# Optimization experiments

Measured on AMD Instinct MI355X. Metric: run time of the kernel, lower is better.

The kernel has to match this reference:

```python
import jax, jax.numpy as jnp
import numpy as np

N, M, D, O = 16384, 4096, 256, 256

def setup_inputs() -> dict:
    key = jax.random.key(0)
    k1, k2, k3, k4, k5, k6, k7 = jax.random.split(key, 7)
    H_fine = jax.random.normal(k1, (N, D), dtype=jnp.float32)
    H_coarse = jax.random.normal(k2, (M, D), dtype=jnp.float32)
    inter_channel_adj = jax.random.randint(k3, (N, M), 0, 2).astype(jnp.float32)
    # attention = nn.Linear(2D, 1): weight vector [2D], bias scalar
    wa = jax.random.normal(k4, (2 * D,), dtype=jnp.float32) * (1.0 / np.sqrt(2 * D))
    ba = jax.random.normal(k5, (1,), dtype=jnp.float32) * 0.01
    # transform = nn.Linear(D, O), xavier_uniform weight
    lim = np.sqrt(6.0 / (D + O)).astype(np.float32)
    Wt = jax.random.uniform(k6, (O, D), minval=-lim, maxval=lim, dtype=jnp.float32)
    bt = jax.random.normal(k7, (O,), dtype=jnp.float32) * 0.01
    return {"H_fine": H_fine, "H_coarse": H_coarse,
            "inter_channel_adj": inter_channel_adj,
            "wa": wa, "ba": ba, "Wt": Wt, "bt": bt}

def reference(H_fine, H_coarse, inter_channel_adj, wa, ba, Wt, bt):
    d = H_fine.shape[-1]
    # additive attention: score_ij = [hf_i ; hc_j] . wa + b
    # = hf_i . wa[:d] + hc_j . wa[d:] + b  (avoids [N,M,2D] concat)
    sf = H_fine @ wa[:d]            # [N]
    sc = H_coarse @ wa[d:]          # [M]
    scores = sf[:, None] + sc[None, :] + ba[0]        # [N, M]
    masked = scores * inter_channel_adj               # [N, M]
    weights = jax.nn.softmax(masked, axis=-1)         # [N, M]
    attn_out = weights @ H_coarse                     # [N, D]
    attn_out = attn_out + H_fine                      # add_self=True
    out = attn_out @ Wt.T + bt                        # [N, O]
    return jax.nn.relu(out)
```

## Files before the change

### kernel.cpp

```cpp
#include <hip/hip_runtime.h>
#include <hip/hip_bf16.h>
#include <stdint.h>

#define N_ 16384
#define M_ 4096
#define D_ 256
#define O_ 256

#define WS_T    0
#define WS_U    65536
#define WS_R    81920
#define WS_WTP  98304
#define WS_BP   229376

typedef float  f32x4  __attribute__((ext_vector_type(4)));
typedef short  short8 __attribute__((ext_vector_type(8)));

__device__ __forceinline__ unsigned short f2bf(float f) {
  uint32_t u = __float_as_uint(f);
  u += 0x7FFFu + ((u >> 16) & 1u);
  return (unsigned short)(u >> 16);
}
__device__ __forceinline__ uint32_t cvtpk(float a, float b) {
  __hip_bfloat162 h = __float22bfloat162_rn(float2{a, b});
  uint32_t u;
  __builtin_memcpy(&u, &h, 4);
  return u;
}

__global__ __launch_bounds__(256) void prep_kernel(
    const float* __restrict__ Hf, const float* __restrict__ Hc,
    const float* __restrict__ wa, const float* __restrict__ ba,
    const float* __restrict__ Wt, float* __restrict__ tv,
    float* __restrict__ uv, unsigned short* __restrict__ BP,
    unsigned short* __restrict__ WtP, float* __restrict__ Rv) {
  __shared__ float tile[64][65];
  __shared__ float red[4][64];
  int b = blockIdx.x;
  int t = threadIdx.x;
  if (b < 5120) {
    int wv = t >> 6, lane = t & 63;
    const float* X; const float* w; const float* bias; float* outv; int row;
    if (b < 4096) { X = Hf; w = wa;      bias = ba;      outv = tv; row = b * 4 + wv; }
    else          { X = Hc; w = wa + D_; bias = nullptr; outv = uv; row = (b - 4096) * 4 + wv; }
    const float4* x4 = (const float4*)(X + (size_t)row * D_);
    const float4* w4 = (const float4*)w;
    float4 xa = x4[lane], wa4 = w4[lane];
    float s = xa.x * wa4.x + xa.y * wa4.y + xa.z * wa4.z + xa.w * wa4.w;
#pragma unroll
    for (int off = 32; off > 0; off >>= 1) s += __shfl_xor(s, off);
    if (lane == 0) outv[row] = expf(s + (bias ? bias[0] : 0.0f));
  } else if (b < 5376) {
    int bb = b - 5120;
    int bk = bb >> 2;
    int bc = bb & 3;
    int k0 = bk * 64, col0 = bc * 64;
    int lane = t & 63, wv = t >> 6;
    int m = lane & 15, q = lane >> 4;
    float colsum = 0.0f;
#pragma unroll
    for (int i = 0; i < 16; ++i) {
      int e = t + 256 * i;
      int kk = e >> 6, cc = e & 63;
      float v = Hc[(size_t)(k0 + kk) * D_ + col0 + cc];
      tile[kk][cc] = v;
      colsum += v;
    }
    red[wv][t & 63] = colsum;
    __syncthreads();
    if (t < 64)
      atomicAdd(&Rv[col0 + t], red[0][t] + red[1][t] + red[2][t] + red[3][t]);
#pragma unroll
    for (int t8 = 0; t8 < 2; ++t8) {
      int tile_id = t8 * 4 + wv;
      int sub = tile_id >> 2, g = tile_id & 3;
      int kgg = bk * 2 + sub;
      int cgg = bc * 4 + g;
      short8 v8;
#pragma unroll
      for (int j = 0; j < 8; ++j)
        v8[j] = (short)f2bf(tile[sub * 32 + q * 8 + j][g * 16 + m]);
      *(short8*)(BP + ((size_t)(kgg * 16 + cgg) * 64 + lane) * 8) = v8;
    }
  } else {
    int tt = (b - 5376) * 256 + t;
    int lane = tt & 63, cg = (tt >> 6) & 15, kg = tt >> 10;
    int m = lane & 15, q = lane >> 4;
    const float* src = Wt + (size_t)(cg * 16 + m) * D_ + kg * 32 + q * 8;
    float4 w0 = *(const float4*)src, w1 = *(const float4*)(src + 4);
    short8 v8;
    v8[0] = (short)f2bf(w0.x); v8[1] = (short)f2bf(w0.y);
    v8[2] = (short)f2bf(w0.z); v8[3] = (short)f2bf(w0.w);
    v8[4] = (short)f2bf(w1.x); v8[5] = (short)f2bf(w1.y);
    v8[6] = (short)f2bf(w1.z); v8[7] = (short)f2bf(w1.w);
    *(short8*)(WtP + (size_t)tt * 8) = v8;
  }
}

__device__ __forceinline__ short8 frag_bits(uint32_t bits, float t,
                                            float4 u0, float4 u1) {
  float c[8];
  c[0] = fmaf(t, u0.x, -1.0f); c[1] = fmaf(t, u0.y, -1.0f);
  c[2] = fmaf(t, u0.z, -1.0f); c[3] = fmaf(t, u0.w, -1.0f);
  c[4] = fmaf(t, u1.x, -1.0f); c[5] = fmaf(t, u1.y, -1.0f);
  c[6] = fmaf(t, u1.z, -1.0f); c[7] = fmaf(t, u1.w, -1.0f);
  union { short8 s; uint32_t u[4]; } r;
#pragma unroll
  for (int p = 0; p < 4; ++p) {
    uint32_t mlo = (uint32_t)((int32_t)(bits << (31 - 2 * p)) >> 31);
    uint32_t mhi = (uint32_t)((int32_t)(bits << (30 - 2 * p)) >> 31);
    r.u[p] = cvtpk(c[2 * p], c[2 * p + 1]) &
             ((mlo & 0x0000FFFFu) | (mhi & 0xFFFF0000u));
  }
  return r.s;
}

__global__ __launch_bounds__(1024, 4) void mega_kernel(
    const float* __restrict__ adj, const unsigned short* __restrict__ BP,
    const float* __restrict__ tv, const float* __restrict__ uv,
    const float* __restrict__ Rv, const float* __restrict__ Hf,
    const unsigned short* __restrict__ WtP, const float* __restrict__ bt,
    float* __restrict__ out) {
  __shared__ __align__(16) char smem[115200];
  unsigned int (*bt2)[129] = (unsigned int (*)[129])(smem);
  float* u_lds = (float*)(smem + 33024);
  float (*Cred)[256] = (float (*)[256])(smem + 49408);
  float* Lsum_lds = (float*)(smem + 114944);
  unsigned short (*attn)[264] = (unsigned short (*)[264])(smem);

  int tid = threadIdx.x;
  int w = tid >> 6, lane = tid & 63;
  int q = lane >> 4, m = lane & 15;
  int colq = w >> 2, ksub = w & 3;
  int i0 = blockIdx.x * 64;

  for (int i = tid; i < M_; i += 1024) u_lds[i] = uv[i];
  __syncthreads();

#pragma unroll 1
  for (int pass = 0; pass < 2; ++pass) {
    int r0 = w * 4 + pass * 2;
    const float* arA = adj + ((size_t)i0 + r0) * M_;
    const float* arB = arA + M_;
    float suA = 0.f, scA = 0.f, suB = 0.f, scB = 0.f;
    float a0 = arA[lane], a1 = arA[64 + lane], a2 = arA[128 + lane], a3 = arA[192 + lane];
    float b0 = arB[lane], b1 = arB[64 + lane], b2 = arB[128 + lane], b3 = arB[192 + lane];
#pragma unroll 1
    for (int i = 0; i < 16; ++i) {
      int k0 = i * 256;
      int k1 = (i + 1 < 16) ? k0 + 256 : 0;
      float na0 = arA[k1 + lane],       na1 = arA[k1 + 64 + lane];
      float na2 = arA[k1 + 128 + lane], na3 = arA[k1 + 192 + lane];
      float nb0 = arB[k1 + lane],       nb1 = arB[k1 + 64 + lane];
      float nb2 = arB[k1 + 128 + lane], nb3 = arB[k1 + 192 + lane];

      unsigned long long wA0 = __ballot(a0 != 0.0f), wA1 = __ballot(a1 != 0.0f);
      unsigned long long wA2 = __ballot(a2 != 0.0f), wA3 = __ballot(a3 != 0.0f);
      unsigned long long wB0 = __ballot(b0 != 0.0f), wB1 = __ballot(b1 != 0.0f);
      unsigned long long wB2 = __ballot(b2 != 0.0f), wB3 = __ballot(b3 != 0.0f);
      suA = fmaf(a0, u_lds[k0 + lane], suA);
      suA = fmaf(a1, u_lds[k0 + 64 + lane], suA);
      suA = fmaf(a2, u_lds[k0 + 128 + lane], suA);
      suA = fmaf(a3, u_lds[k0 + 192 + lane], suA);
      scA += (a0 + a1) + (a2 + a3);
      suB = fmaf(b0, u_lds[k0 + lane], suB);
      suB = fmaf(b1, u_lds[k0 + 64 + lane], suB);
      suB = fmaf(b2, u_lds[k0 + 128 + lane], suB);
      suB = fmaf(b3, u_lds[k0 + 192 + lane], suB);
      scB += (b0 + b1) + (b2 + b3);
      if (lane < 16) {
        int rowsel = lane >> 3;
        int c = (lane >> 1) & 3, hi = lane & 1;
        unsigned long long v = rowsel ? (c == 0 ? wB0 : c == 1 ? wB1 : c == 2 ? wB2 : wB3)
                                      : (c == 0 ? wA0 : c == 1 ? wA1 : c == 2 ? wA2 : wA3);
        bt2[r0 + rowsel][i * 8 + c * 2 + hi] =
            hi ? (unsigned int)(v >> 32) : (unsigned int)v;
      }
      a0 = na0; a1 = na1; a2 = na2; a3 = na3;
      b0 = nb0; b1 = nb1; b2 = nb2; b3 = nb3;
    }
#pragma unroll
    for (int off = 32; off > 0; off >>= 1) {
      suA += __shfl_xor(suA, off); scA += __shfl_xor(scA, off);
      suB += __shfl_xor(suB, off); scB += __shfl_xor(scB, off);
    }
    if (lane == 0) {
      Lsum_lds[r0]     = tv[i0 + r0] * suA - scA;
      Lsum_lds[r0 + 1] = tv[i0 + r0 + 1] * suB - scB;
    }
  }

  const unsigned short* bbase = BP + (size_t)(colq * 4) * 512 + (size_t)lane * 8;
  int kg0 = ksub * 32;
  short8 curB[4];
#pragma unroll
  for (int n = 0; n < 4; ++n)
    curB[n] = *(const short8*)(bbase + ((size_t)kg0 * 16 + n) * 512);
  float t0 = tv[i0 + m], t1 = tv[i0 + 16 + m];
  float t2 = tv[i0 + 32 + m], t3 = tv[i0 + 48 + m];

  f32x4 acc[4][4];
#pragma unroll
  for (int s = 0; s < 4; ++s)
#pragma unroll
    for (int n = 0; n < 4; ++n) acc[s][n] = (f32x4){0.f, 0.f, 0.f, 0.f};

  __syncthreads();

  for (int it = 0; it < 32; ++it) {
    int kg = kg0 + it;
    int kn = (it + 1 < 32) ? kg + 1 : kg0;
    short8 nB[4];
#pragma unroll
    for (int n = 0; n < 4; ++n)
      nB[n] = *(const short8*)(bbase + ((size_t)kn * 16 + n) * 512);

    float4 u0 = *(const float4*)&u_lds[kg * 32 + q * 8];
    float4 u1 = *(const float4*)&u_lds[kg * 32 + q * 8 + 4];
    uint32_t b0 = bt2[m][kg],      b1 = bt2[16 + m][kg];
    uint32_t b2 = bt2[32 + m][kg], b3 = bt2[48 + m][kg];
    int sh = q * 8;
    short8 af0 = frag_bits((b0 >> sh) & 0xffu, t0, u0, u1);
    short8 af1 = frag_bits((b1 >> sh) & 0xffu, t1, u0, u1);
    short8 af2 = frag_bits((b2 >> sh) & 0xffu, t2, u0, u1);
    short8 af3 = frag_bits((b3 >> sh) & 0xffu, t3, u0, u1);
#pragma unroll
    for (int n = 0; n < 4; ++n) {
      acc[0][n] = __builtin_amdgcn_mfma_f32_16x16x32_bf16(af0, curB[n], acc[0][n], 0, 0, 0);
      acc[1][n] = __builtin_amdgcn_mfma_f32_16x16x32_bf16(af1, curB[n], acc[1][n], 0, 0, 0);
      acc[2][n] = __builtin_amdgcn_mfma_f32_16x16x32_bf16(af2, curB[n], acc[2][n], 0, 0, 0);
      acc[3][n] = __builtin_amdgcn_mfma_f32_16x16x32_bf16(af3, curB[n], acc[3][n], 0, 0, 0);
    }
#pragma unroll
    for (int n = 0; n < 4; ++n) curB[n] = nB[n];
  }

#pragma unroll
  for (int s4 = 0; s4 < 4; ++s4) {
    if (ksub == s4) {
#pragma unroll
      for (int s = 0; s < 4; ++s)
#pragma unroll
        for (int n = 0; n < 4; ++n) {
          int col = colq * 64 + n * 16 + m;
#pragma unroll
          for (int r = 0; r < 4; ++r) {
            int rl = s * 16 + q * 4 + r;
            if (s4 == 0) Cred[rl][col] = acc[s][n][r];
            else         Cred[rl][col] += acc[s][n][r];
          }
        }
    }
    __syncthreads();
  }

  {
    int row = tid >> 4;
    int c0 = (tid & 15) * 16;
    size_t grow = (size_t)i0 + row;
    float invL = 1.0f / (Lsum_lds[row] + (float)M_);
    const float* hfp = Hf + grow * D_ + c0;
    const float* rvp = Rv + c0;
    const float* crp = &Cred[row][c0];
#pragma unroll
    for (int g = 0; g < 4; ++g) {
      float4 cv = *(const float4*)(crp + g * 4);
      float4 rv = *(const float4*)(rvp + g * 4);
      float4 hv = *(const float4*)(hfp + g * 4);
      float v0 = fmaf(cv.x + rv.x, invL, hv.x);
      float v1 = fmaf(cv.y + rv.y, invL, hv.y);
      float v2 = fmaf(cv.z + rv.z, invL, hv.z);
      float v3 = fmaf(cv.w + rv.w, invL, hv.w);
      *(uint32_t*)&attn[row][c0 + g * 4]     = cvtpk(v0, v1);
      *(uint32_t*)&attn[row][c0 + g * 4 + 2] = cvtpk(v2, v3);
    }
  }
  __syncthreads();

  {
    int rt = w & 3, cq = w >> 2;
    f32x4 facc[4];
#pragma unroll
    for (int n = 0; n < 4; ++n) facc[n] = (f32x4){0.f, 0.f, 0.f, 0.f};
    const unsigned short* wwave = WtP + (size_t)(cq * 4) * 512 + (size_t)lane * 8;
#pragma unroll
    for (int kf = 0; kf < 8; ++kf) {
      short8 af = *(const short8*)&attn[rt * 16 + m][kf * 32 + q * 8];
#pragma unroll
      for (int n = 0; n < 4; ++n) {
        short8 bf = *(const short8*)(wwave + ((size_t)kf * 16 + n) * 512);
        facc[n] = __builtin_amdgcn_mfma_f32_16x16x32_bf16(af, bf, facc[n], 0, 0, 0);
      }
    }
#pragma unroll
    for (int n = 0; n < 4; ++n) {
      int col = cq * 64 + n * 16 + m;
      float b = bt[col];
#pragma unroll
      for (int r = 0; r < 4; ++r) {
        size_t row = (size_t)i0 + rt * 16 + q * 4 + r;
        out[row * O_ + col] = fmaxf(facc[n][r] + b, 0.0f);
      }
    }
  }
}

extern "C" void kernel_launch(void* const* d_in, const int* in_sizes, int n_in,
                              void* d_out, int out_size, void* d_ws, size_t ws_size,
                              hipStream_t stream) {
  const float* Hf  = (const float*)d_in[0];
  const float* Hc  = (const float*)d_in[1];
  const float* adj = (const float*)d_in[2];
  const float* wa  = (const float*)d_in[3];
  const float* ba  = (const float*)d_in[4];
  const float* Wt  = (const float*)d_in[5];
  const float* bt  = (const float*)d_in[6];
  float* out = (float*)d_out;

  char* ws = (char*)d_ws;
  float* tv   = (float*)(ws + WS_T);
  float* uv   = (float*)(ws + WS_U);
  float* Rv   = (float*)(ws + WS_R);
  unsigned short* WtP = (unsigned short*)(ws + WS_WTP);
  unsigned short* BP  = (unsigned short*)(ws + WS_BP);

  hipMemsetAsync(Rv, 0, D_ * sizeof(float), stream);

  prep_kernel<<<5408, 256, 0, stream>>>(Hf, Hc, wa, ba, Wt, tv, uv, BP, WtP, Rv);
  mega_kernel<<<256, 1024, 0, stream>>>(adj, BP, tv, uv, Rv, Hf, WtP, bt, out);
}
```

Measured before the change: 462.4 us.

## Switch attention MFMAs from bf16 to fp16 with packed half2 fragment generation

Converts all packed operands and MFMA calls from bf16 to fp16, and builds the A fragments with packed half2 FMAs (t*u-1) from a precomputed half2 copy of u in LDS. This replaces eight fp32 FMAs plus bf16 pack conversions per fragment. The main loop is also manually unrolled by two with ping-pong B register buffers, and bit-mask words are read as uint2. This cuts VALU work in the fragment-generation hot loop, at the cost of fp16 range and precision for t*u products and the attention output. LDS usage also grows slightly.

Result: faster. 440.8 us (-4.7%).

```diff
diff --git a/kernel.cpp b/kernel.cpp
--- a/kernel.cpp
+++ b/kernel.cpp
@@ -1,5 +1,5 @@
 #include <hip/hip_runtime.h>
-#include <hip/hip_bf16.h>
+#include <hip/hip_fp16.h>
 #include <stdint.h>
 
 #define N_ 16384
@@ -14,15 +14,16 @@
 #define WS_BP   229376
 
 typedef float  f32x4  __attribute__((ext_vector_type(4)));
-typedef short  short8 __attribute__((ext_vector_type(8)));
-
-__device__ __forceinline__ unsigned short f2bf(float f) {
-  uint32_t u = __float_as_uint(f);
-  u += 0x7FFFu + ((u >> 16) & 1u);
-  return (unsigned short)(u >> 16);
-}
-__device__ __forceinline__ uint32_t cvtpk(float a, float b) {
-  __hip_bfloat162 h = __float22bfloat162_rn(float2{a, b});
+typedef _Float16 half8 __attribute__((ext_vector_type(8)));
+
+__device__ __forceinline__ unsigned short f2h(float f) {
+  __half h = __float2half(f);
+  unsigned short u;
+  __builtin_memcpy(&u, &h, 2);
+  return u;
+}
+__device__ __forceinline__ uint32_t hpack(float a, float b) {
+  __half2 h = __floats2half2_rn(a, b);
   uint32_t u;
   __builtin_memcpy(&u, &h, 4);
   return u;
@@ -76,11 +77,11 @@
       int sub = tile_id >> 2, g = tile_id & 3;
       int kgg = bk * 2 + sub;
       int cgg = bc * 4 + g;
-      short8 v8;
+      unsigned short v8[8];
 #pragma unroll
       for (int j = 0; j < 8; ++j)
-        v8[j] = (short)f2bf(tile[sub * 32 + q * 8 + j][g * 16 + m]);
-      *(short8*)(BP + ((size_t)(kgg * 16 + cgg) * 64 + lane) * 8) = v8;
+        v8[j] = f2h(tile[sub * 32 + q * 8 + j][g * 16 + m]);
+      *(uint4*)(BP + ((size_t)(kgg * 16 + cgg) * 64 + lane) * 8) = *(uint4*)v8;
     }
   } else {
     int tt = (b - 5376) * 256 + t;
@@ -88,31 +89,26 @@
     int m = lane & 15, q = lane >> 4;
     const float* src = Wt + (size_t)(cg * 16 + m) * D_ + kg * 32 + q * 8;
     float4 w0 = *(const float4*)src, w1 = *(const float4*)(src + 4);
-    short8 v8;
-    v8[0] = (short)f2bf(w0.x); v8[1] = (short)f2bf(w0.y);
-    v8[2] = (short)f2bf(w0.z); v8[3] = (short)f2bf(w0.w);
-    v8[4] = (short)f2bf(w1.x); v8[5] = (short)f2bf(w1.y);
-    v8[6] = (short)f2bf(w1.z); v8[7] = (short)f2bf(w1.w);
-    *(short8*)(WtP + (size_t)tt * 8) = v8;
-  }
-}
-
-__device__ __forceinline__ short8 frag_bits(uint32_t bits, float t,
-                                            float4 u0, float4 u1) {
-  float c[8];
-  c[0] = fmaf(t, u0.x, -1.0f); c[1] = fmaf(t, u0.y, -1.0f);
-  c[2] = fmaf(t, u0.z, -1.0f); c[3] = fmaf(t, u0.w, -1.0f);
-  c[4] = fmaf(t, u1.x, -1.0f); c[5] = fmaf(t, u1.y, -1.0f);
-  c[6] = fmaf(t, u1.z, -1.0f); c[7] = fmaf(t, u1.w, -1.0f);
-  union { short8 s; uint32_t u[4]; } r;
+    unsigned short v8[8];
+    v8[0] = f2h(w0.x); v8[1] = f2h(w0.y); v8[2] = f2h(w0.z); v8[3] = f2h(w0.w);
+    v8[4] = f2h(w1.x); v8[5] = f2h(w1.y); v8[6] = f2h(w1.z); v8[7] = f2h(w1.w);
+    *(uint4*)(WtP + (size_t)tt * 8) = *(uint4*)v8;
+  }
+}
+
+__device__ __forceinline__ half8 frag_f16(uint32_t bits, __half2 th,
+                                          const __half2* up, __half2 mone) {
+  union { half8 h; uint32_t u[4]; } r;
 #pragma unroll
   for (int p = 0; p < 4; ++p) {
+    __half2 v = __hfma2(th, up[p], mone);
+    uint32_t c;
+    __builtin_memcpy(&c, &v, 4);
     uint32_t mlo = (uint32_t)((int32_t)(bits << (31 - 2 * p)) >> 31);
     uint32_t mhi = (uint32_t)((int32_t)(bits << (30 - 2 * p)) >> 31);
-    r.u[p] = cvtpk(c[2 * p], c[2 * p + 1]) &
-             ((mlo & 0x0000FFFFu) | (mhi & 0xFFFF0000u));
-  }
-  return r.s;
+    r.u[p] = c & ((mlo & 0x0000FFFFu) | (mhi & 0xFFFF0000u));
+  }
+  return r.h;
 }
 
 __global__ __launch_bounds__(1024, 4) void mega_kernel(
@@ -121,11 +117,12 @@
     const float* __restrict__ Rv, const float* __restrict__ Hf,
     const unsigned short* __restrict__ WtP, const float* __restrict__ bt,
     float* __restrict__ out) {
-  __shared__ __align__(16) char smem[115200];
-  unsigned int (*bt2)[129] = (unsigned int (*)[129])(smem);
-  float* u_lds = (float*)(smem + 33024);
-  float (*Cred)[256] = (float (*)[256])(smem + 49408);
-  float* Lsum_lds = (float*)(smem + 114944);
+  __shared__ __align__(16) char smem[123648];
+  unsigned int (*bt2)[130] = (unsigned int (*)[130])(smem);
+  float* u_lds = (float*)(smem + 33280);
+  uint32_t* u_h2 = (uint32_t*)(smem + 49664);
+  float (*Cred)[256] = (float (*)[256])(smem + 57856);
+  float* Lsum_lds = (float*)(smem + 123392);
   unsigned short (*attn)[264] = (unsigned short (*)[264])(smem);
 
   int tid = threadIdx.x;
@@ -134,7 +131,11 @@
   int colq = w >> 2, ksub = w & 3;
   int i0 = blockIdx.x * 64;
 
-  for (int i = tid; i < M_; i += 1024) u_lds[i] = uv[i];
+  for (int i = tid; i < M_ / 2; i += 1024) {
+    float2 u2 = *(const float2*)(uv + 2 * i);
+    u_lds[2 * i] = u2.x; u_lds[2 * i + 1] = u2.y;
+    u_h2[i] = hpack(u2.x, u2.y);
+  }
   __syncthreads();
 
 #pragma unroll 1
@@ -192,12 +193,16 @@
 
   const unsigned short* bbase = BP + (size_t)(colq * 4) * 512 + (size_t)lane * 8;
   int kg0 = ksub * 32;
-  short8 curB[4];
+  half8 bufA[4], bufB[4];
 #pragma unroll
   for (int n = 0; n < 4; ++n)
-    curB[n] = *(const short8*)(bbase + ((size_t)kg0 * 16 + n) * 512);
-  float t0 = tv[i0 + m], t1 = tv[i0 + 16 + m];
-  float t2 = tv[i0 + 32 + m], t3 = tv[i0 + 48 + m];
+    bufA[n] = *(const half8*)(bbase + ((size_t)kg0 * 16 + n) * 512);
+
+  __half2 th0 = __float2half2_rn(tv[i0 + m]);
+  __half2 th1 = __float2half2_rn(tv[i0 + 16 + m]);
+  __half2 th2 = __float2half2_rn(tv[i0 + 32 + m]);
+  __half2 th3 = __float2half2_rn(tv[i0 + 48 + m]);
+  const __half2 mone = __float2half2_rn(-1.0f);
 
   f32x4 acc[4][4];
 #pragma unroll
@@ -207,32 +212,67 @@
 
   __syncthreads();
 
-  for (int it = 0; it < 32; ++it) {
-    int kg = kg0 + it;
-    int kn = (it + 1 < 32) ? kg + 1 : kg0;
-    short8 nB[4];
+#pragma unroll 1
+  for (int it2 = 0; it2 < 16; ++it2) {
+    int kg = kg0 + it2 * 2;
+    uint2 W0 = *(const uint2*)&bt2[m][kg];
+    uint2 W1 = *(const uint2*)&bt2[16 + m][kg];
+    uint2 W2 = *(const uint2*)&bt2[32 + m][kg];
+    uint2 W3 = *(const uint2*)&bt2[48 + m][kg];
+    int sh = q * 8;
+
 #pragma unroll
     for (int n = 0; n < 4; ++n)
-      nB[n] = *(const short8*)(bbase + ((size_t)kn * 16 + n) * 512);
-
-    float4 u0 = *(const float4*)&u_lds[kg * 32 + q * 8];
-    float4 u1 = *(const float4*)&u_lds[kg * 32 + q * 8 + 4];
-    uint32_t b0 = bt2[m][kg],      b1 = bt2[16 + m][kg];
-    uint32_t b2 = bt2[32 + m][kg], b3 = bt2[48 + m][kg];
-    int sh = q * 8;
-    short8 af0 = frag_bits((b0 >> sh) & 0xffu, t0, u0, u1);
-    short8 af1 = frag_bits((b1 >> sh) & 0xffu, t1, u0, u1);
-    short8 af2 = frag_bits((b2 >> sh) & 0xffu, t2, u0, u1);
-    short8 af3 = frag_bits((b3 >> sh) & 0xffu, t3, u0, u1);
-#pragma unroll
-    for (int n = 0; n < 4; ++n) {
-      acc[0][n] = __builtin_amdgcn_mfma_f32_16x16x32_bf16(af0, curB[n], acc[0][n], 0, 0, 0);
-      acc[1][n] = __builtin_amdgcn_mfma_f32_16x16x32_bf16(af1, curB[n], acc[1][n], 0, 0, 0);
-      acc[2][n] = __builtin_amdgcn_mfma_f32_16x16x32_bf16(af2, curB[n], acc[2][n], 0, 0, 0);
-      acc[3][n] = __builtin_amdgcn_mfma_f32_16x16x32_bf16(af3, curB[n], acc[3][n], 0, 0, 0);
-    }
-#pragma unroll
-    for (int n = 0; n < 4; ++n) curB[n] = nB[n];
+      bufB[n] = *(const half8*)(bbase + ((size_t)(kg + 1) * 16 + n) * 512);
+    {
+      uint4 uu = *(const uint4*)&u_h2[kg * 16 + q * 4];
+      __half2 up[4];
+      __builtin_memcpy(up, &uu, 16);
+      half8 af;
+      af = frag_f16((W0.x >> sh) & 0xffu, th0, up, mone);
+#pragma unroll
+      for (int n = 0; n < 4; ++n)
+        acc[0][n] = __builtin_amdgcn_mfma_f32_16x16x32_f16(af, bufA[n], acc[0][n], 0, 0, 0);
+      af = frag_f16((W1.x >> sh) & 0xffu, th1, up, mone);
+#pragma unroll
+      for (int n = 0; n < 4; ++n)
+        acc[1][n] = __builtin_amdgcn_mfma_f32_16x16x32_f16(af, bufA[n], acc[1][n], 0, 0, 0);
+      af = frag_f16((W2.x >> sh) & 0xffu, th2, up, mone);
+#pragma unroll
+      for (int n = 0; n < 4; ++n)
+        acc[2][n] = __builtin_amdgcn_mfma_f32_16x16x32_f16(af, bufA[n], acc[2][n], 0, 0, 0);
+      af = frag_f16((W3.x >> sh) & 0xffu, th3, up, mone);
+#pragma unroll
+      for (int n = 0; n < 4; ++n)
+        acc[3][n] = __builtin_amdgcn_mfma_f32_16x16x32_f16(af, bufA[n], acc[3][n], 0, 0, 0);
+    }
+
+    int kn = (it2 + 1 < 16) ? kg + 2 : kg0;
+#pragma unroll
+    for (int n = 0; n < 4; ++n)
+      bufA[n] = *(const half8*)(bbase + ((size_t)kn * 16 + n) * 512);
+    {
+      uint4 uu = *(const uint4*)&u_h2[(kg + 1) * 16 + q * 4];
+      __half2 up[4];
+      __builtin_memcpy(up, &uu, 16);
+      half8 af;
+      af = frag_f16((W0.y >> sh) & 0xffu, th0, up, mone);
+#pragma unroll
+      for (int n = 0; n < 4; ++n)
+        acc[0][n] = __builtin_amdgcn_mfma_f32_16x16x32_f16(af, bufB[n], acc[0][n], 0, 0, 0);
+      af = frag_f16((W1.y >> sh) & 0xffu, th1, up, mone);
+#pragma unroll
+      for (int n = 0; n < 4; ++n)
+        acc[1][n] = __builtin_amdgcn_mfma_f32_16x16x32_f16(af, bufB[n], acc[1][n], 0, 0, 0);
+      af = frag_f16((W2.y >> sh) & 0xffu, th2, up, mone);
+#pragma unroll
+      for (int n = 0; n < 4; ++n)
+        acc[2][n] = __builtin_amdgcn_mfma_f32_16x16x32_f16(af, bufB[n], acc[2][n], 0, 0, 0);
+      af = frag_f16((W3.y >> sh) & 0xffu, th3, up, mone);
+#pragma unroll
+      for (int n = 0; n < 4; ++n)
+        acc[3][n] = __builtin_amdgcn_mfma_f32_16x16x32_f16(af, bufB[n], acc[3][n], 0, 0, 0);
+    }
   }
 
 #pragma unroll
@@ -271,8 +311,8 @@
       float v1 = fmaf(cv.y + rv.y, invL, hv.y);
       float v2 = fmaf(cv.z + rv.z, invL, hv.z);
       float v3 = fmaf(cv.w + rv.w, invL, hv.w);
-      *(uint32_t*)&attn[row][c0 + g * 4]     = cvtpk(v0, v1);
-      *(uint32_t*)&attn[row][c0 + g * 4 + 2] = cvtpk(v2, v3);
+      *(uint32_t*)&attn[row][c0 + g * 4]     = hpack(v0, v1);
+      *(uint32_t*)&attn[row][c0 + g * 4 + 2] = hpack(v2, v3);
     }
   }
   __syncthreads();
@@ -285,11 +325,11 @@
     const unsigned short* wwave = WtP + (size_t)(cq * 4) * 512 + (size_t)lane * 8;
 #pragma unroll
     for (int kf = 0; kf < 8; ++kf) {
-      short8 af = *(const short8*)&attn[rt * 16 + m][kf * 32 + q * 8];
+      half8 af = *(const half8*)&attn[rt * 16 + m][kf * 32 + q * 8];
 #pragma unroll
       for (int n = 0; n < 4; ++n) {
-        short8 bf = *(const short8*)(wwave + ((size_t)kf * 16 + n) * 512);
-        facc[n] = __builtin_amdgcn_mfma_f32_16x16x32_bf16(af, bf, facc[n], 0, 0, 0);
+        half8 bf = *(const half8*)(wwave + ((size_t)kf * 16 + n) * 512);
+        facc[n] = __builtin_amdgcn_mfma_f32_16x16x32_f16(af, bf, facc[n], 0, 0, 0);
       }
     }
 #pragma unroll
```
